# Optimization experiments

Measured on AMD Instinct MI355X. Metric: run time of the kernel, lower is better.

Reference implementation:

```python
import jax, jax.numpy as jnp
import numpy as np

N_HEADS = 16
D_EMBED = 1024
D_HEAD = D_EMBED // N_HEADS
CAUSAL = False


def setup_inputs() -> dict:
    key = jax.random.key(0)
    k1, k2, k3, k4, k5 = jax.random.split(key, 5)
    B, S, D = 4, 2048, D_EMBED
    scale = 1.0 / np.sqrt(D)
    return {
        "x": jax.random.normal(k1, (B, S, D), dtype=jnp.float32),
        "w_in": jax.random.normal(k2, (D, 3 * D), dtype=jnp.float32) * scale,
        "b_in": jax.random.normal(k3, (3 * D,), dtype=jnp.float32) * 0.02,
        "w_out": jax.random.normal(k4, (D, D), dtype=jnp.float32) * scale,
        "b_out": jax.random.normal(k5, (D,), dtype=jnp.float32) * 0.02,
    }


def reference(x, w_in, b_in, w_out, b_out):
    B, S, D = x.shape
    qkv = jnp.einsum("bsd,de->bse", x, w_in) + b_in  # [B,S,3D]
    q, k, v = jnp.split(qkv, 3, axis=-1)
    # split heads -> [B,H,S,Dh]
    def sh(t):
        return t.reshape(B, S, N_HEADS, D_HEAD).transpose(0, 2, 1, 3)
    q, k, v = sh(q), sh(k), sh(v)
    weight = jnp.einsum("bhsd,bhtd->bhst", q, k)  # [B,H,S,S]
    if CAUSAL:
        mask = jnp.triu(jnp.ones((S, S), dtype=bool), k=1)
        weight = jnp.where(mask, -jnp.inf, weight)
    weight = weight / np.sqrt(D_HEAD)
    weight = jax.nn.softmax(weight, axis=-1)
    out = jnp.einsum("bhst,bhtd->bhsd", weight, v)
    out = out.transpose(0, 2, 1, 3).reshape(B, S, D)
    return jnp.einsum("bsd,de->bse", out, w_out) + b_out
```

## Files before the change

### kernel.cpp

```cpp
#include <hip/hip_runtime.h>
#include <hip/hip_bf16.h>

typedef unsigned short u16;
typedef __attribute__((ext_vector_type(8))) short bf16x8;
typedef __attribute__((ext_vector_type(4))) float f32x4;
typedef __attribute__((ext_vector_type(16))) float f32x16;

#define QSCALE 0.180336880f

#define DEV static __device__ __forceinline__

DEV u16 f2bf(float f) {
  union { float f; unsigned u; } v; v.f = f;
  unsigned r = v.u + 0x7fffu + ((v.u >> 16) & 1u);
  return (u16)(r >> 16);
}

DEV unsigned pk2(float a, float b) {
  union { __hip_bfloat162 h; unsigned u; } c;
  c.h = __float22bfloat162_rn(make_float2(a, b));
  return c.u;
}

DEV void gll16(void* lds, const void* g) {
  __builtin_amdgcn_global_load_lds(
      (const __attribute__((address_space(1))) unsigned int*)g,
      (__attribute__((address_space(3))) unsigned int*)lds, 16, 0, 0);
}

__global__ __launch_bounds__(256) void cvt_f32_to_bf16(const float* __restrict__ in,
                                                       u16* __restrict__ out, int n4) {
  int i = blockIdx.x * blockDim.x + threadIdx.x;
  int stride = gridDim.x * blockDim.x;
  for (; i < n4; i += stride) {
    float4 f = ((const float4*)in)[i];
    ushort4 u;
    u.x = f2bf(f.x); u.y = f2bf(f.y); u.z = f2bf(f.z); u.w = f2bf(f.w);
    ((ushort4*)out)[i] = u;
  }
}

__global__ __launch_bounds__(256) void transpose_cvt(const float* __restrict__ W,
                                                     u16* __restrict__ Wt,
                                                     int K, int N, int sn, float sval) {
  __shared__ u16 t[64][65];
  const int k0 = blockIdx.x * 64, n0 = blockIdx.y * 64;
  const int tid = threadIdx.x;
  const int rr = tid >> 4;
  const int cc = (tid & 15) * 4;
  const float scl = (n0 < sn) ? sval : 1.0f;
#pragma unroll
  for (int i = 0; i < 4; ++i) {
    const int row = rr * 4 + i;
    float4 f = *(const float4*)&W[(size_t)(k0 + row) * N + n0 + cc];
    t[row][cc + 0] = f2bf(f.x * scl);
    t[row][cc + 1] = f2bf(f.y * scl);
    t[row][cc + 2] = f2bf(f.z * scl);
    t[row][cc + 3] = f2bf(f.w * scl);
  }
  __syncthreads();
#pragma unroll
  for (int i = 0; i < 4; ++i) {
    const int n = rr * 4 + i;
    ushort4 u;
    u.x = t[cc + 0][n]; u.y = t[cc + 1][n]; u.z = t[cc + 2][n]; u.w = t[cc + 3][n];
    *(ushort4*)&Wt[(size_t)(n0 + n) * K + k0 + cc] = u;
  }
}

__global__ __launch_bounds__(256) void transpose_v(const u16* __restrict__ qkv,
                                                   u16* __restrict__ vT) {
  __shared__ u16 t[64][72];
  const int bh = blockIdx.y;
  const int b = bh >> 4, h = bh & 15;
  const int t0 = blockIdx.x * 64;
  const int tid = threadIdx.x;
  const int row = tid >> 2;
  const int cg = (tid & 3) * 16;
  const size_t src = (size_t)b * 2048 * 3072 + (size_t)(t0 + row) * 3072 + 2048 + h * 64 + cg;
  bf16x8 v0 = *(const bf16x8*)&qkv[src];
  bf16x8 v1 = *(const bf16x8*)&qkv[src + 8];
#pragma unroll
  for (int i = 0; i < 8; ++i) { t[row][cg + i] = (u16)v0[i]; t[row][cg + 8 + i] = (u16)v1[i]; }
  __syncthreads();
  const int d = tid >> 2;
  const int tg = (tid & 3) * 16;
  bf16x8 o0, o1;
#pragma unroll
  for (int i = 0; i < 8; ++i) { o0[i] = (short)t[tg + i][d]; o1[i] = (short)t[tg + 8 + i][d]; }
  u16* dst = &vT[((size_t)bh * 64 + d) * 2048 + t0 + tg];
  *(bf16x8*)dst = o0;
  *(bf16x8*)(dst + 8) = o1;
}


#define G1_STAGE(S)                                                   \
  {                                                                   \
    gll16((u16*)L1[S] + wave * 512, g0); g0 += 32;                    \
    gll16((u16*)L1[S] + 4096 + wave * 512, g1); g1 += 32;             \
    gll16((u16*)L1[S] + 8192 + wave * 512, g2); g2 += 32;             \
    gll16((u16*)L1[S] + 12288 + wave * 512, g3); g3 += 32;            \
  }

#define G1_BODY(S, ISSUE, VM)                                         \
  {                                                                   \
    if (ISSUE) G1_STAGE((S + 2) & 3)                                  \
    asm volatile("s_waitcnt vmcnt(" #VM ")" ::: "memory");            \
    __builtin_amdgcn_s_barrier();                                     \
    const char* sb = (const char*)L1[S];                              \
    bf16x8 af[8], bfr[4];                                             \
    _Pragma("unroll")                                                 \
    for (int m = 0; m < 8; ++m) af[m] = *(const bf16x8*)(sb + aoff[m]); \
    _Pragma("unroll")                                                 \
    for (int n = 0; n < 4; ++n) bfr[n] = *(const bf16x8*)(sb + boff[n]); \
    __builtin_amdgcn_s_setprio(1);                                    \
    _Pragma("unroll")                                                 \
    for (int m = 0; m < 8; ++m)                                       \
      _Pragma("unroll")                                               \
      for (int n = 0; n < 4; ++n)                                     \
        acc[m][n] = __builtin_amdgcn_mfma_f32_16x16x32_bf16(af[m], bfr[n], acc[m][n], 0, 0, 0); \
    __builtin_amdgcn_s_setprio(0);                                    \
  }

__global__ __launch_bounds__(512, 2) void gemm1_256(const u16* __restrict__ A,
                                                    const u16* __restrict__ Bt,
                                                    const float* __restrict__ bias,
                                                    u16* __restrict__ C) {
  __shared__ __align__(16) u16 L1[4][16384];
  const int tid = threadIdx.x;
  const int wave = tid >> 6, lane = tid & 63;
  const int g = lane >> 4, lr = lane & 15;
  const int wr = wave >> 2, wc = wave & 3;
  const int id = blockIdx.x;
  const int xcd = id & 7, j = id >> 3;
  const int bm = (xcd * 4 + (j & 3)) * 256;
  const int bn = (j >> 2) * 256;

  int aoff[8], boff[4];
#pragma unroll
  for (int m = 0; m < 8; ++m)
    aoff[m] = wr * 8192 + m * 1024 + g * 256 + lr * 16;
#pragma unroll
  for (int n = 0; n < 4; ++n)
    boff[n] = 16384 + wc * 4096 + n * 1024 + g * 256 + lr * 16;

  const u16* g0; const u16* g1; const u16* g2; const u16* g3;
  {
    const int b0 = wave * 1024 + lane * 16;
    const int plane = b0 >> 8, lrr = (b0 >> 4) & 15, pb = b0 & 15;
    const int row = (plane >> 2) * 16 + lrr;
    const int kc = (plane & 3) * 8 + (pb >> 1);
    g0 = A  + (size_t)(bm + row) * 1024 + kc;
    g1 = A  + (size_t)(bm + 128 + row) * 1024 + kc;
    g2 = Bt + (size_t)(bn + row) * 1024 + kc;
    g3 = Bt + (size_t)(bn + 128 + row) * 1024 + kc;
  }

  f32x4 acc[8][4] = {};

  G1_STAGE(0)
  G1_STAGE(1)

  for (int it = 0; it < 7; ++it) {
    G1_BODY(0, 1, 8) G1_BODY(1, 1, 8) G1_BODY(2, 1, 8) G1_BODY(3, 1, 8)
  }
  G1_BODY(0, 1, 8)
  G1_BODY(1, 1, 8)
  G1_BODY(2, 0, 4)
  G1_BODY(3, 0, 0)

#pragma unroll
  for (int m = 0; m < 8; ++m) {
#pragma unroll
    for (int n = 0; n < 4; ++n) {
      const int col = bn + wc * 64 + n * 16 + lr;
      float bv = bias[col];
      if (col < 1024) bv *= QSCALE;
#pragma unroll
      for (int r = 0; r < 4; ++r) {
        const int row = bm + wr * 128 + m * 16 + g * 4 + r;
        C[(size_t)row * 3072 + col] = f2bf(acc[m][n][r] + bv);
      }
    }
  }
}

template<bool OUT_BF16>
__global__ __launch_bounds__(256) void gemm_bf16(const u16* __restrict__ A,
                                                 const u16* __restrict__ Bt,
                                                 const float* __restrict__ bias,
                                                 void* __restrict__ Cout,
                                                 int M, int N, int K, int qn) {
  __shared__ __align__(16) u16 As[128][64];
  __shared__ __align__(16) u16 Bs[128][64];
  const int tid = threadIdx.x;
  const int wave = tid >> 6, lane = tid & 63;
  const int g = lane >> 4, lr = lane & 15;
  const int lid = blockIdx.y * gridDim.x + blockIdx.x;
  const int chunk = gridDim.x >> 3;
  const int xcd = lid & 7, j = lid >> 3;
  const int bm = (xcd * chunk + (j % chunk)) * 128;
  const int bn = (j / chunk) * 128;
  const int wm = (wave >> 1) * 64, wn = (wave & 1) * 64;
  f32x4 acc[4][4] = {};
  for (int kt = 0; kt < K; kt += 64) {
    __syncthreads();
#pragma unroll
    for (int jj = 0; jj < 4; ++jj) {
      int chnk = wave * 4 + jj;
      int e = chnk * 512 + lane * 8;
      int r = e >> 6, c = e & 63;
      gll16((u16*)As + chnk * 512, &A[(size_t)(bm + r) * K + kt + c]);
      gll16((u16*)Bs + chnk * 512, &Bt[(size_t)(bn + r) * K + kt + c]);
    }
    __syncthreads();
#pragma unroll
    for (int kk = 0; kk < 64; kk += 32) {
      bf16x8 af[4], bfr[4];
#pragma unroll
      for (int m = 0; m < 4; ++m)
        af[m] = *(const bf16x8*)&As[wm + m * 16 + lr][kk + g * 8];
#pragma unroll
      for (int n = 0; n < 4; ++n)
        bfr[n] = *(const bf16x8*)&Bs[wn + n * 16 + lr][kk + g * 8];
#pragma unroll
      for (int m = 0; m < 4; ++m)
#pragma unroll
        for (int n = 0; n < 4; ++n)
          acc[m][n] = __builtin_amdgcn_mfma_f32_16x16x32_bf16(af[m], bfr[n], acc[m][n], 0, 0, 0);
    }
  }
#pragma unroll
  for (int m = 0; m < 4; ++m) {
#pragma unroll
    for (int n = 0; n < 4; ++n) {
      const int col = bn + wn + n * 16 + lr;
      float bv = bias ? bias[col] : 0.f;
      if (col < qn) bv *= QSCALE;
#pragma unroll
      for (int r = 0; r < 4; ++r) {
        const int row = bm + wm + m * 16 + g * 4 + r;
        float v = acc[m][n][r] + bv;
        if (OUT_BF16) ((u16*)Cout)[(size_t)row * N + col] = f2bf(v);
        else          ((float*)Cout)[(size_t)row * N + col] = v;
      }
    }
  }
}


#define ATTN_BODY(BUF, ISSUE, VM)                                                 \
  {                                                                               \
    if (ISSUE) {                                                                  \
      gll16((u16*)Ks[((BUF) + 2) & 3] + wave * 512, gk); gk += 32 * 3072;         \
      gll16((u16*)Vs[((BUF) + 2) & 3] + wave * 512, gv); gv += 32;                \
    }                                                                             \
    asm volatile("s_waitcnt vmcnt(" #VM ")" ::: "memory");                        \
    __builtin_amdgcn_s_barrier();                                                 \
    const char* kb = (const char*)Ks[(BUF)];                                      \
    const char* vb = (const char*)Vs[(BUF)];                                      \
    f32x16 s = {};                                                                \
    __builtin_amdgcn_s_setprio(1);                                                \
    _Pragma("unroll")                                                             \
    for (int kk = 0; kk < 4; ++kk) {                                              \
      bf16x8 kf = *(const bf16x8*)(kb + koff[kk]);                                \
      s = __builtin_amdgcn_mfma_f32_32x32x16_bf16(kf, qf[kk], s, 0, 0, 0);        \
    }                                                                             \
    __builtin_amdgcn_s_setprio(0);                                                \
    float pr[16];                                                                 \
    _Pragma("unroll")                                                             \
    for (int r = 0; r < 16; ++r) pr[r] = __builtin_amdgcn_exp2f(s[r]);            \
    lsum += ((pr[0] + pr[1]) + (pr[2] + pr[3])) + ((pr[4] + pr[5]) + (pr[6] + pr[7])) \
          + ((pr[8] + pr[9]) + (pr[10] + pr[11])) + ((pr[12] + pr[13]) + (pr[14] + pr[15])); \
    union { unsigned u[4]; bf16x8 v; } pa0, pa1;                                  \
    {                                                                             \
      unsigned X0 = pk2(pr[0], pr[1]), X1 = pk2(pr[2], pr[3]);                    \
      unsigned Y0 = pk2(pr[4], pr[5]), Y1 = pk2(pr[6], pr[7]);                    \
      asm volatile("v_permlane32_swap_b32 %0, %1" : "+v"(X0), "+v"(Y0));          \
      asm volatile("v_permlane32_swap_b32 %0, %1" : "+v"(X1), "+v"(Y1));          \
      pa0.u[0] = X0; pa0.u[1] = X1; pa0.u[2] = Y0; pa0.u[3] = Y1;                 \
      unsigned Z0 = pk2(pr[8], pr[9]), Z1 = pk2(pr[10], pr[11]);                  \
      unsigned W0 = pk2(pr[12], pr[13]), W1 = pk2(pr[14], pr[15]);                \
      asm volatile("v_permlane32_swap_b32 %0, %1" : "+v"(Z0), "+v"(W0));          \
      asm volatile("v_permlane32_swap_b32 %0, %1" : "+v"(Z1), "+v"(W1));          \
      pa1.u[0] = Z0; pa1.u[1] = Z1; pa1.u[2] = W0; pa1.u[3] = W1;                 \
    }                                                                             \
    __builtin_amdgcn_s_setprio(1);                                                \
    {                                                                             \
      bf16x8 vf00 = *(const bf16x8*)(vb + voff[0][0]);                            \
      bf16x8 vf10 = *(const bf16x8*)(vb + voff[1][0]);                            \
      o0 = __builtin_amdgcn_mfma_f32_32x32x16_bf16(pa0.v, vf00, o0, 0, 0, 0);     \
      o1 = __builtin_amdgcn_mfma_f32_32x32x16_bf16(pa0.v, vf10, o1, 0, 0, 0);     \
      bf16x8 vf01 = *(const bf16x8*)(vb + voff[0][1]);                            \
      bf16x8 vf11 = *(const bf16x8*)(vb + voff[1][1]);                            \
      o0 = __builtin_amdgcn_mfma_f32_32x32x16_bf16(pa1.v, vf01, o0, 0, 0, 0);     \
      o1 = __builtin_amdgcn_mfma_f32_32x32x16_bf16(pa1.v, vf11, o1, 0, 0, 0);     \
    }                                                                             \
    __builtin_amdgcn_s_setprio(0);                                                \
  }

__global__ __launch_bounds__(256, 4) void attn_kernel(const u16* __restrict__ qkv,
                                                      const u16* __restrict__ vT,
                                                      u16* __restrict__ out) {
  __shared__ __align__(16) u16 Ks[4][2048];
  __shared__ __align__(16) u16 Vs[4][2048];
  const int tid = threadIdx.x;
  const int wave = tid >> 6, lane = tid & 63;
  const int hi = lane >> 5, l31 = lane & 31;
  const int id = blockIdx.x;
  const int bh = ((id >> 3) & 7) * 8 + (id & 7);
  const int b = bh >> 4, h = bh & 15;
  const int q0 = (id >> 6) * 128;
  const size_t base = (size_t)b * 2048 * 3072;
  const u16* kg = qkv + base + 1024 + h * 64;
  const u16* vg = vT + (size_t)bh * 64 * 2048;

  const int qrow = q0 + wave * 32 + l31;
  bf16x8 qf[4];
#pragma unroll
  for (int kk = 0; kk < 4; ++kk)
    qf[kk] = *(const bf16x8*)&qkv[base + (size_t)qrow * 3072 + h * 64 + kk * 16 + hi * 8];

  int koff[4];
#pragma unroll
  for (int kk = 0; kk < 4; ++kk)
    koff[kk] = (kk * 2 + hi) * 512 + l31 * 16;
  int voff[2][2];
#pragma unroll
  for (int dt = 0; dt < 2; ++dt)
#pragma unroll
    for (int kp = 0; kp < 2; ++kp)
      voff[dt][kp] = (dt * 4 + kp * 2 + hi) * 512 + l31 * 16;

  const u16* gk = kg + (size_t)l31 * 3072 + wave * 16 + hi * 8;
  const u16* gv = vg + (size_t)((wave >> 1) * 32 + l31) * 2048 + (wave & 1) * 16 + hi * 8;

  f32x16 o0 = {}, o1 = {};
  float lsum = 0.f;

  gll16((u16*)Ks[0] + wave * 512, gk); gk += 32 * 3072;
  gll16((u16*)Vs[0] + wave * 512, gv); gv += 32;
  gll16((u16*)Ks[1] + wave * 512, gk); gk += 32 * 3072;
  gll16((u16*)Vs[1] + wave * 512, gv); gv += 32;

  for (int it4 = 0; it4 < 15; ++it4) {
    ATTN_BODY(0, true, 4)
    ATTN_BODY(1, true, 4)
    ATTN_BODY(2, true, 4)
    ATTN_BODY(3, true, 4)
  }
  ATTN_BODY(0, true, 4)
  ATTN_BODY(1, true, 4)
  ATTN_BODY(2, false, 2)
  ATTN_BODY(3, false, 0)

  float lt = lsum + __shfl_xor(lsum, 32);
  const size_t orow0 = (size_t)b * 2048 + q0 + wave * 32;
#pragma unroll
  for (int r = 0; r < 16; ++r) {
    const int crow = (r & 3) + 8 * (r >> 2) + 4 * hi;
    const float li = __shfl(lt, crow);
    u16* orow = out + (orow0 + crow) * 1024 + h * 64 + l31;
    orow[0]  = f2bf(o0[r] / li);
    orow[32] = f2bf(o1[r] / li);
  }
}

extern "C" void kernel_launch(void* const* d_in, const int* in_sizes, int n_in,
                              void* d_out, int out_size, void* d_ws, size_t ws_size,
                              hipStream_t stream) {
  (void)in_sizes; (void)n_in; (void)out_size; (void)ws_size;
  const float* x     = (const float*)d_in[0];
  const float* w_in  = (const float*)d_in[1];
  const float* b_in  = (const float*)d_in[2];
  const float* w_out = (const float*)d_in[3];
  const float* b_out = (const float*)d_in[4];
  float* out = (float*)d_out;

  char* ws = (char*)d_ws;
  u16* Xbf   = (u16*)ws; ws += (size_t)8192 * 1024 * 2;
  u16* WinT  = (u16*)ws; ws += (size_t)3072 * 1024 * 2;
  u16* WoutT = (u16*)ws; ws += (size_t)1024 * 1024 * 2;
  u16* qkv   = (u16*)ws; ws += (size_t)8192 * 3072 * 2;
  u16* attno = (u16*)ws;
  u16* vT    = Xbf;

  cvt_f32_to_bf16<<<2048, 256, 0, stream>>>(x, Xbf, 8192 * 1024 / 4);
  transpose_cvt<<<dim3(16, 48), 256, 0, stream>>>(w_in, WinT, 1024, 3072, 1024, QSCALE);
  transpose_cvt<<<dim3(16, 16), 256, 0, stream>>>(w_out, WoutT, 1024, 1024, 0, 1.0f);
  gemm1_256<<<384, 512, 0, stream>>>(Xbf, WinT, b_in, qkv);
  transpose_v<<<dim3(32, 64), 256, 0, stream>>>(qkv, vT);
  attn_kernel<<<1024, 256, 0, stream>>>(qkv, vT, attno);
  gemm_bf16<false><<<dim3(64, 8), 256, 0, stream>>>(attno, WoutT, b_out, out, 8192, 1024, 1024, 0);
}
```

Baseline: 223.3 us.

## Split attention KV range across two wave groups per block and merge via LDS

```diff
diff --git a/kernel.cpp b/kernel.cpp
--- a/kernel.cpp
+++ b/kernel.cpp
@@ -249,16 +249,14 @@
 }
 
 
-#define ATTN_BODY(BUF, ISSUE, VM)                                                 \
+#define ATTN_BODY(S, ISSUE)                                                       \
   {                                                                               \
     if (ISSUE) {                                                                  \
-      gll16((u16*)Ks[((BUF) + 2) & 3] + wave * 512, gk); gk += 32 * 3072;         \
-      gll16((u16*)Vs[((BUF) + 2) & 3] + wave * 512, gv); gv += 32;                \
+      gll16(Kb + ((S) ^ 1) * 2048 + w4 * 512, gk); gk += 32 * 3072;               \
+      gll16(Vb + ((S) ^ 1) * 2048 + w4 * 512, gv); gv += 32;                      \
     }                                                                             \
-    asm volatile("s_waitcnt vmcnt(" #VM ")" ::: "memory");                        \
-    __builtin_amdgcn_s_barrier();                                                 \
-    const char* kb = (const char*)Ks[(BUF)];                                      \
-    const char* vb = (const char*)Vs[(BUF)];                                      \
+    const char* kb = (const char*)(Kb + (S) * 2048);                              \
+    const char* vb = (const char*)(Vb + (S) * 2048);                              \
     f32x16 s = {};                                                                \
     __builtin_amdgcn_s_setprio(1);                                                \
     _Pragma("unroll")                                                             \
@@ -297,25 +295,27 @@
       o1 = __builtin_amdgcn_mfma_f32_32x32x16_bf16(pa1.v, vf11, o1, 0, 0, 0);     \
     }                                                                             \
     __builtin_amdgcn_s_setprio(0);                                                \
-  }
-
-__global__ __launch_bounds__(256, 4) void attn_kernel(const u16* __restrict__ qkv,
+    asm volatile("s_waitcnt vmcnt(0)" ::: "memory");                              \
+    __builtin_amdgcn_s_barrier();                                                 \
+  }
+
+__global__ __launch_bounds__(512, 8) void attn_kernel(const u16* __restrict__ qkv,
                                                       const u16* __restrict__ vT,
                                                       u16* __restrict__ out) {
-  __shared__ __align__(16) u16 Ks[4][2048];
-  __shared__ __align__(16) u16 Vs[4][2048];
+  __shared__ __align__(16) u16 lds[16896];
   const int tid = threadIdx.x;
-  const int wave = tid >> 6, lane = tid & 63;
+  const int g8 = tid >> 6, lane = tid & 63;
+  const int grp = g8 >> 2, w4 = g8 & 3;
   const int hi = lane >> 5, l31 = lane & 31;
   const int id = blockIdx.x;
   const int bh = ((id >> 3) & 7) * 8 + (id & 7);
   const int b = bh >> 4, h = bh & 15;
-  const int q0 = (id >> 6) * 128;
+  const int q0i = (id >> 6) * 128;
   const size_t base = (size_t)b * 2048 * 3072;
   const u16* kg = qkv + base + 1024 + h * 64;
   const u16* vg = vT + (size_t)bh * 64 * 2048;
 
-  const int qrow = q0 + wave * 32 + l31;
+  const int qrow = q0i + w4 * 32 + l31;
   bf16x8 qf[4];
 #pragma unroll
   for (int kk = 0; kk < 4; ++kk)
@@ -332,37 +332,57 @@
     for (int kp = 0; kp < 2; ++kp)
       voff[dt][kp] = (dt * 4 + kp * 2 + hi) * 512 + l31 * 16;
 
-  const u16* gk = kg + (size_t)l31 * 3072 + wave * 16 + hi * 8;
-  const u16* gv = vg + (size_t)((wave >> 1) * 32 + l31) * 2048 + (wave & 1) * 16 + hi * 8;
+  u16* Kb = lds + grp * 8192;
+  u16* Vb = lds + grp * 8192 + 4096;
+
+  const u16* gk = kg + (size_t)(grp * 1024 + l31) * 3072 + w4 * 16 + hi * 8;
+  const u16* gv = vg + (size_t)((w4 >> 1) * 32 + l31) * 2048 + grp * 1024
+                + (w4 & 1) * 16 + hi * 8;
 
   f32x16 o0 = {}, o1 = {};
   float lsum = 0.f;
 
-  gll16((u16*)Ks[0] + wave * 512, gk); gk += 32 * 3072;
-  gll16((u16*)Vs[0] + wave * 512, gv); gv += 32;
-  gll16((u16*)Ks[1] + wave * 512, gk); gk += 32 * 3072;
-  gll16((u16*)Vs[1] + wave * 512, gv); gv += 32;
-
-  for (int it4 = 0; it4 < 15; ++it4) {
-    ATTN_BODY(0, true, 4)
-    ATTN_BODY(1, true, 4)
-    ATTN_BODY(2, true, 4)
-    ATTN_BODY(3, true, 4)
-  }
-  ATTN_BODY(0, true, 4)
-  ATTN_BODY(1, true, 4)
-  ATTN_BODY(2, false, 2)
-  ATTN_BODY(3, false, 0)
-
-  float lt = lsum + __shfl_xor(lsum, 32);
-  const size_t orow0 = (size_t)b * 2048 + q0 + wave * 32;
-#pragma unroll
-  for (int r = 0; r < 16; ++r) {
-    const int crow = (r & 3) + 8 * (r >> 2) + 4 * hi;
-    const float li = __shfl(lt, crow);
-    u16* orow = out + (orow0 + crow) * 1024 + h * 64 + l31;
-    orow[0]  = f2bf(o0[r] / li);
-    orow[32] = f2bf(o1[r] / li);
+  gll16(Kb + w4 * 512, gk); gk += 32 * 3072;
+  gll16(Vb + w4 * 512, gv); gv += 32;
+  asm volatile("s_waitcnt vmcnt(0)" ::: "memory");
+  __builtin_amdgcn_s_barrier();
+
+  for (int it = 0; it < 15; ++it) { ATTN_BODY(0, 1) ATTN_BODY(1, 1) }
+  ATTN_BODY(0, 1)
+  ATTN_BODY(1, 0)
+
+  if (grp == 1) {
+    char* ob = (char*)lds + w4 * 8192;
+#pragma unroll
+    for (int rq = 0; rq < 4; ++rq) {
+      f32x4 u0 = { o0[rq * 4 + 0], o0[rq * 4 + 1], o0[rq * 4 + 2], o0[rq * 4 + 3] };
+      f32x4 u1 = { o1[rq * 4 + 0], o1[rq * 4 + 1], o1[rq * 4 + 2], o1[rq * 4 + 3] };
+      *(f32x4*)(ob + rq * 1024 + lane * 16) = u0;
+      *(f32x4*)(ob + 4096 + rq * 1024 + lane * 16) = u1;
+    }
+    ((float*)((char*)lds + 32768))[w4 * 64 + lane] = lsum;
+  }
+  __syncthreads();
+  if (grp == 0) {
+    const float lB = ((const float*)((const char*)lds + 32768))[w4 * 64 + lane];
+    const float ls = lsum + lB;
+    const float lt = ls + __shfl_xor(ls, 32);
+    const char* ob = (const char*)lds + w4 * 8192;
+    const size_t orow0 = (size_t)b * 2048 + q0i + w4 * 32;
+#pragma unroll
+    for (int rq = 0; rq < 4; ++rq) {
+      f32x4 u0 = *(const f32x4*)(ob + rq * 1024 + lane * 16);
+      f32x4 u1 = *(const f32x4*)(ob + 4096 + rq * 1024 + lane * 16);
+#pragma unroll
+      for (int jj = 0; jj < 4; ++jj) {
+        const int r = rq * 4 + jj;
+        const int crow = jj + 8 * rq + 4 * hi;
+        const float li = __shfl(lt, crow);
+        u16* orow = out + (orow0 + crow) * 1024 + h * 64 + l31;
+        orow[0]  = f2bf((o0[r] + u0[jj]) / li);
+        orow[32] = f2bf((o1[r] + u1[jj]) / li);
+      }
+    }
   }
 }
 
@@ -390,6 +410,6 @@
   transpose_cvt<<<dim3(16, 16), 256, 0, stream>>>(w_out, WoutT, 1024, 1024, 0, 1.0f);
   gemm1_256<<<384, 512, 0, stream>>>(Xbf, WinT, b_in, qkv);
   transpose_v<<<dim3(32, 64), 256, 0, stream>>>(qkv, vT);
-  attn_kernel<<<1024, 256, 0, stream>>>(qkv, vT, attno);
+  attn_kernel<<<1024, 512, 0, stream>>>(qkv, vT, attno);
   gemm_bf16<false><<<dim3(64, 8), 256, 0, stream>>>(attno, WoutT, b_out, out, 8192, 1024, 1024, 0);
 }
```

Result: slower. 686.4 us (+207.4%).

## Software-pipeline QK^T one tile ahead of softmax/PV in attention loop

Applied to the files above, without the earlier changes.

```diff
diff --git a/kernel.cpp b/kernel.cpp
--- a/kernel.cpp
+++ b/kernel.cpp
@@ -249,27 +249,30 @@
 }
 
 
-#define ATTN_BODY(BUF, ISSUE, VM)                                                 \
+#define ATTN_T15(SLOT, SFIN, SQK, ISS, VM, DOQK)                                  \
   {                                                                               \
-    if (ISSUE) {                                                                  \
-      gll16((u16*)Ks[((BUF) + 2) & 3] + wave * 512, gk); gk += 32 * 3072;         \
-      gll16((u16*)Vs[((BUF) + 2) & 3] + wave * 512, gv); gv += 32;                \
-    }                                                                             \
     asm volatile("s_waitcnt vmcnt(" #VM ")" ::: "memory");                        \
     __builtin_amdgcn_s_barrier();                                                 \
-    const char* kb = (const char*)Ks[(BUF)];                                      \
-    const char* vb = (const char*)Vs[(BUF)];                                      \
-    f32x16 s = {};                                                                \
-    __builtin_amdgcn_s_setprio(1);                                                \
-    _Pragma("unroll")                                                             \
-    for (int kk = 0; kk < 4; ++kk) {                                              \
-      bf16x8 kf = *(const bf16x8*)(kb + koff[kk]);                                \
-      s = __builtin_amdgcn_mfma_f32_32x32x16_bf16(kf, qf[kk], s, 0, 0, 0);        \
+    if (ISS) {                                                                    \
+      gll16((u16*)Ks[((SLOT) + 3) & 3] + wave * 512, gk); gk += 32 * 3072;        \
+      gll16((u16*)Vs[((SLOT) + 3) & 3] + wave * 512, gv); gv += 32;               \
     }                                                                             \
-    __builtin_amdgcn_s_setprio(0);                                                \
+    if (DOQK) {                                                                   \
+      const char* kb = (const char*)Ks[((SLOT) + 1) & 3];                         \
+      _Pragma("unroll")                                                           \
+      for (int r = 0; r < 16; ++r) SQK[r] = 0.f;                                  \
+      __builtin_amdgcn_s_setprio(1);                                              \
+      _Pragma("unroll")                                                           \
+      for (int kk = 0; kk < 4; ++kk) {                                            \
+        bf16x8 kf = *(const bf16x8*)(kb + pob + kk * 1024);                       \
+        SQK = __builtin_amdgcn_mfma_f32_32x32x16_bf16(kf, qf[kk], SQK, 0, 0, 0);  \
+      }                                                                           \
+      __builtin_amdgcn_s_setprio(0);                                              \
+    }                                                                             \
+    const char* vb = (const char*)Vs[(SLOT)];                                     \
     float pr[16];                                                                 \
     _Pragma("unroll")                                                             \
-    for (int r = 0; r < 16; ++r) pr[r] = __builtin_amdgcn_exp2f(s[r]);            \
+    for (int r = 0; r < 16; ++r) pr[r] = __builtin_amdgcn_exp2f(SFIN[r]);         \
     lsum += ((pr[0] + pr[1]) + (pr[2] + pr[3])) + ((pr[4] + pr[5]) + (pr[6] + pr[7])) \
           + ((pr[8] + pr[9]) + (pr[10] + pr[11])) + ((pr[12] + pr[13]) + (pr[14] + pr[15])); \
     union { unsigned u[4]; bf16x8 v; } pa0, pa1;                                  \
@@ -287,12 +290,12 @@
     }                                                                             \
     __builtin_amdgcn_s_setprio(1);                                                \
     {                                                                             \
-      bf16x8 vf00 = *(const bf16x8*)(vb + voff[0][0]);                            \
-      bf16x8 vf10 = *(const bf16x8*)(vb + voff[1][0]);                            \
+      bf16x8 vf00 = *(const bf16x8*)(vb + pob);                                   \
+      bf16x8 vf10 = *(const bf16x8*)(vb + pob + 2048);                            \
       o0 = __builtin_amdgcn_mfma_f32_32x32x16_bf16(pa0.v, vf00, o0, 0, 0, 0);     \
       o1 = __builtin_amdgcn_mfma_f32_32x32x16_bf16(pa0.v, vf10, o1, 0, 0, 0);     \
-      bf16x8 vf01 = *(const bf16x8*)(vb + voff[0][1]);                            \
-      bf16x8 vf11 = *(const bf16x8*)(vb + voff[1][1]);                            \
+      bf16x8 vf01 = *(const bf16x8*)(vb + pob + 1024);                            \
+      bf16x8 vf11 = *(const bf16x8*)(vb + pob + 3072);                            \
       o0 = __builtin_amdgcn_mfma_f32_32x32x16_bf16(pa1.v, vf01, o0, 0, 0, 0);     \
       o1 = __builtin_amdgcn_mfma_f32_32x32x16_bf16(pa1.v, vf11, o1, 0, 0, 0);     \
     }                                                                             \
@@ -321,38 +324,47 @@
   for (int kk = 0; kk < 4; ++kk)
     qf[kk] = *(const bf16x8*)&qkv[base + (size_t)qrow * 3072 + h * 64 + kk * 16 + hi * 8];
 
-  int koff[4];
-#pragma unroll
-  for (int kk = 0; kk < 4; ++kk)
-    koff[kk] = (kk * 2 + hi) * 512 + l31 * 16;
-  int voff[2][2];
-#pragma unroll
-  for (int dt = 0; dt < 2; ++dt)
-#pragma unroll
-    for (int kp = 0; kp < 2; ++kp)
-      voff[dt][kp] = (dt * 4 + kp * 2 + hi) * 512 + l31 * 16;
+  const int pob = hi * 512 + l31 * 16;
 
   const u16* gk = kg + (size_t)l31 * 3072 + wave * 16 + hi * 8;
   const u16* gv = vg + (size_t)((wave >> 1) * 32 + l31) * 2048 + (wave & 1) * 16 + hi * 8;
 
   f32x16 o0 = {}, o1 = {};
   float lsum = 0.f;
+  f32x16 sA, sB;
 
   gll16((u16*)Ks[0] + wave * 512, gk); gk += 32 * 3072;
   gll16((u16*)Vs[0] + wave * 512, gv); gv += 32;
   gll16((u16*)Ks[1] + wave * 512, gk); gk += 32 * 3072;
   gll16((u16*)Vs[1] + wave * 512, gv); gv += 32;
-
-  for (int it4 = 0; it4 < 15; ++it4) {
-    ATTN_BODY(0, true, 4)
-    ATTN_BODY(1, true, 4)
-    ATTN_BODY(2, true, 4)
-    ATTN_BODY(3, true, 4)
-  }
-  ATTN_BODY(0, true, 4)
-  ATTN_BODY(1, true, 4)
-  ATTN_BODY(2, false, 2)
-  ATTN_BODY(3, false, 0)
+  gll16((u16*)Ks[2] + wave * 512, gk); gk += 32 * 3072;
+  gll16((u16*)Vs[2] + wave * 512, gv); gv += 32;
+  asm volatile("s_waitcnt vmcnt(4)" ::: "memory");
+  __builtin_amdgcn_s_barrier();
+
+  {
+    const char* kb = (const char*)Ks[0];
+#pragma unroll
+    for (int r = 0; r < 16; ++r) sA[r] = 0.f;
+    __builtin_amdgcn_s_setprio(1);
+#pragma unroll
+    for (int kk = 0; kk < 4; ++kk) {
+      bf16x8 kf = *(const bf16x8*)(kb + pob + kk * 1024);
+      sA = __builtin_amdgcn_mfma_f32_32x32x16_bf16(kf, qf[kk], sA, 0, 0, 0);
+    }
+    __builtin_amdgcn_s_setprio(0);
+  }
+
+  for (int it = 0; it < 15; ++it) {
+    ATTN_T15(0, sA, sB, 1, 2, 1)
+    ATTN_T15(1, sB, sA, 1, 2, 1)
+    ATTN_T15(2, sA, sB, 1, 2, 1)
+    ATTN_T15(3, sB, sA, 1, 2, 1)
+  }
+  ATTN_T15(0, sA, sB, 1, 2, 1)
+  ATTN_T15(1, sB, sA, 0, 2, 1)
+  ATTN_T15(2, sA, sB, 0, 0, 1)
+  ATTN_T15(3, sB, sA, 0, 0, 0)
 
   float lt = lsum + __shfl_xor(lsum, 32);
   const size_t orow0 = (size_t)b * 2048 + q0 + wave * 32;
```

After: 224.4 us. About the same (+0.5%).
